# Performance work log

Measured on AMD Instinct MI355X. Metric: run time of the kernel, lower is better.

The kernel has to match this reference:

```python
import jax, jax.numpy as jnp
import numpy as np

B, C, N = 4, 512, 2048
H, DK = 8, 64  # n_heads, d_k; H*DK == C


def setup_inputs() -> dict:
    key = jax.random.key(0)
    k1, k2, k3 = jax.random.split(key, 3)
    x = jax.random.normal(k1, (B, C, N), dtype=jnp.float32)
    # Linear(C, 3*H*DK) and Linear(H*DK, C); torch Linear weight is [out, in]
    Wp = jax.random.normal(k2, (3 * H * DK, C), dtype=jnp.float32) * (C ** -0.5)
    bp = jnp.zeros((3 * H * DK,), dtype=jnp.float32)
    Wo = jax.random.normal(k3, (C, H * DK), dtype=jnp.float32) * ((H * DK) ** -0.5)
    bo = jnp.zeros((C,), dtype=jnp.float32)
    return {"x": x, "Wp": Wp, "bp": bp, "Wo": Wo, "bo": bo}


def reference(x, Wp, bp, Wo, bo):
    b, c, n = x.shape
    scale = DK ** -0.5
    xt = jnp.transpose(x, (0, 2, 1))                    # [b, n, c]
    # NOTE: original forward never applies self.norm (GroupNorm) — faithful omission.
    qkv = xt @ Wp.T + bp                                # [b, n, 3*H*DK]
    qkv = qkv.reshape(b, n, H, 3 * DK)
    q, k, v = jnp.split(qkv, 3, axis=-1)                # each [b, n, H, DK]
    attn = jnp.einsum('bihd,bjhd->bijh', q, k) * scale  # [b, n, n, H]
    attn = jax.nn.softmax(attn, axis=1)                 # softmax over QUERY axis (nonstandard)
    res = jnp.einsum('bijh,bjhd->bihd', attn, v)        # [b, n, H, DK]
    res = res.reshape(b, n, H * DK)
    res = res @ Wo.T + bo                               # [b, n, c]
    res = res + xt                                      # shortcut = Identity (in==out)
    return jnp.transpose(res, (0, 2, 1)).reshape(b, c, n)
```

## Files before the change

### kernel.cpp

```cpp
#include <hip/hip_runtime.h>
#include <cstddef>

typedef unsigned short ushort_t;
typedef __attribute__((ext_vector_type(8))) short sh8;
typedef __attribute__((ext_vector_type(4))) float f4;
typedef __attribute__((ext_vector_type(4))) unsigned short us4;

static constexpr int Bc = 4, Cc = 512, Nc = 2048, Hc = 8, DKc = 64, O3c = 1536;
static constexpr int BHN = Bc * Hc * Nc;
static constexpr int NSPLIT_S = 2;
static constexpr float K2 = 0.125f * 1.44269504089f;

__device__ __forceinline__ unsigned short f2bf(float f) {
    union { float f; unsigned u; } v; v.f = f;
    unsigned r = v.u + 0x7FFFu + ((v.u >> 16) & 1u);
    return (unsigned short)(r >> 16);
}
__device__ __forceinline__ float bf2f(unsigned short b) {
    union { unsigned u; float f; } v; v.u = ((unsigned)b) << 16;
    return v.f;
}
__device__ __forceinline__ float ubf(unsigned u) {
    union { unsigned u; float f; } v; v.u = u; return v.f;
}
__device__ __forceinline__ float fexp2(float s) {
    return ubf((unsigned)(int)fmaf(s, 8388608.0f, 1065353216.0f));
}
__device__ __forceinline__ int fexp2_bf(float s) {
    return (int)fmaf(s, 128.0f, 16256.5f);
}
__device__ __forceinline__ void gl_lds16(const ushort_t* g, ushort_t* l) {
    __builtin_amdgcn_global_load_lds(
        (const __attribute__((address_space(1))) unsigned int*)g,
        (__attribute__((address_space(3))) unsigned int*)l, 16, 0, 0);
}

__global__ __launch_bounds__(256) void xpose_kernel(
    const float* __restrict__ x, ushort_t* __restrict__ xt)
{
    __shared__ float t[32][33];
    const int b = blockIdx.z, n0 = blockIdx.x * 32, c0 = blockIdx.y * 32;
    const int tx = threadIdx.x & 31, ty = threadIdx.x >> 5;
    const float* xb = x + (size_t)b * Cc * Nc;
#pragma unroll
    for (int r = 0; r < 4; ++r)
        t[ty + r * 8][tx] = xb[(size_t)(c0 + ty + r * 8) * Nc + n0 + tx];
    __syncthreads();
    ushort_t* xtb = xt + (size_t)b * Nc * Cc;
#pragma unroll
    for (int r = 0; r < 4; ++r)
        xtb[(size_t)(n0 + ty + r * 8) * Cc + c0 + tx] = f2bf(t[tx][ty + r * 8]);
}

__global__ __launch_bounds__(256) void cvt_kernel(
    const float* __restrict__ s, ushort_t* __restrict__ d, int n4)
{
    int i = blockIdx.x * 256 + threadIdx.x;
    if (i < n4) {
        float4 v = ((const float4*)s)[i];
        us4 o = { f2bf(v.x), f2bf(v.y), f2bf(v.z), f2bf(v.w) };
        ((us4*)d)[i] = o;
    }
}

__global__ __launch_bounds__(256) void qkv_kernel(
    const ushort_t* __restrict__ xt, const ushort_t* __restrict__ Wpb,
    const float* __restrict__ bp,
    ushort_t* __restrict__ q, ushort_t* __restrict__ k, ushort_t* __restrict__ vT)
{
    const int tid = threadIdx.x;
    const int wave = tid >> 6, lane = tid & 63, quad = lane >> 4, l15 = lane & 15;
    const int b = blockIdx.z;
    const int m0 = blockIdx.y * 128 + (wave & 1) * 64;
    const int o0 = blockIdx.x * 128 + (wave >> 1) * 64;
    const ushort_t* A  = xt  + ((size_t)b * Nc + m0) * Cc;
    const ushort_t* Bp = Wpb + (size_t)o0 * Cc;

    const int f  = (o0 >> 6) % 3;
    const int h  = o0 / 192;
    const int bh = b * Hc + h;

    f4 acc[4][4];
#pragma unroll
    for (int i = 0; i < 4; ++i)
#pragma unroll
        for (int j = 0; j < 4; ++j) acc[i][j] = (f4)0.f;

    if (f == 2) {
        for (int kk = 0; kk < Cc; kk += 32) {
            sh8 a[4], bb[4];
#pragma unroll
            for (int mi = 0; mi < 4; ++mi)
                a[mi] = *(const sh8*)&A[(size_t)(mi * 16 + l15) * Cc + kk + quad * 8];
#pragma unroll
            for (int ni = 0; ni < 4; ++ni)
                bb[ni] = *(const sh8*)&Bp[(size_t)(ni * 16 + l15) * Cc + kk + quad * 8];
#pragma unroll
            for (int mi = 0; mi < 4; ++mi)
#pragma unroll
                for (int ni = 0; ni < 4; ++ni)
                    acc[mi][ni] = __builtin_amdgcn_mfma_f32_16x16x32_bf16(
                        a[mi], bb[ni], acc[mi][ni], 0, 0, 0);
        }
#pragma unroll
        for (int ni = 0; ni < 4; ++ni) {
            const int o = o0 + ni * 16 + l15;
            const int d = o & 63;
            const float bias = bp[o];
            ushort_t* dst = vT + ((size_t)bh * DKc + d) * Nc + m0;
#pragma unroll
            for (int mi = 0; mi < 4; ++mi) {
                us4 pk = { f2bf(acc[mi][ni][0] + bias), f2bf(acc[mi][ni][1] + bias),
                           f2bf(acc[mi][ni][2] + bias), f2bf(acc[mi][ni][3] + bias) };
                *(us4*)&dst[mi * 16 + quad * 4] = pk;
            }
        }
    } else {
        for (int kk = 0; kk < Cc; kk += 32) {
            sh8 a[4], bb[4];
#pragma unroll
            for (int mi = 0; mi < 4; ++mi)
                a[mi] = *(const sh8*)&A[(size_t)(mi * 16 + l15) * Cc + kk + quad * 8];
#pragma unroll
            for (int ni = 0; ni < 4; ++ni)
                bb[ni] = *(const sh8*)&Bp[(size_t)(ni * 16 + l15) * Cc + kk + quad * 8];
#pragma unroll
            for (int mo = 0; mo < 4; ++mo)
#pragma unroll
                for (int nt = 0; nt < 4; ++nt)
                    acc[mo][nt] = __builtin_amdgcn_mfma_f32_16x16x32_bf16(
                        bb[mo], a[nt], acc[mo][nt], 0, 0, 0);
        }
        const float qs = (f == 0) ? K2 : 1.0f;
        ushort_t* dst = (f == 0 ? q : k) + (size_t)bh * Nc * DKc;
#pragma unroll
        for (int mo = 0; mo < 4; ++mo) {
            const int d0 = mo * 16 + quad * 4;
            const float4 b4 = *(const float4*)&bp[o0 + d0];
#pragma unroll
            for (int nt = 0; nt < 4; ++nt) {
                const int token = m0 + nt * 16 + l15;
                us4 pk = { f2bf((acc[mo][nt][0] + b4.x) * qs),
                           f2bf((acc[mo][nt][1] + b4.y) * qs),
                           f2bf((acc[mo][nt][2] + b4.z) * qs),
                           f2bf((acc[mo][nt][3] + b4.w) * qs) };
                *(us4*)&dst[(size_t)token * DKc + d0] = pk;
            }
        }
    }
}

__global__ __launch_bounds__(256, 2) void stats_kernel(
    const ushort_t* __restrict__ q, const ushort_t* __restrict__ k,
    float* __restrict__ spart)
{
    const int tid = threadIdx.x;
    const int wave = tid >> 6, lane = tid & 63, quad = lane >> 4, l15 = lane & 15;
    const int id = blockIdx.x;
    const int jb = id >> 6;
    const int bh = (id & 63) >> 1;
    const int js = id & 1;
    const int j0 = jb * 256 + wave * 64;
    const int ibase = js * (Nc / NSPLIT_S);
    const ushort_t* K = k + ((size_t)bh * Nc + j0) * DKc;
    const ushort_t* Q = q + (size_t)bh * Nc * DKc;

    sh8 aK[4][2];
#pragma unroll
    for (int mj = 0; mj < 4; ++mj)
#pragma unroll
        for (int kk = 0; kk < 2; ++kk)
            aK[mj][kk] = *(const sh8*)&K[(size_t)(mj * 16 + l15) * DKc + kk * 32 + quad * 8];

    float lsum[4][4] = {};
    for (int it = 0; it < Nc / NSPLIT_S; it += 64) {
        const int i0 = ibase + it;
        sh8 bQ[4][2];
#pragma unroll
        for (int ni = 0; ni < 4; ++ni)
#pragma unroll
            for (int kk = 0; kk < 2; ++kk)
                bQ[ni][kk] = *(const sh8*)&Q[(size_t)(i0 + ni * 16 + l15) * DKc + kk * 32 + quad * 8];
#pragma unroll
        for (int mj = 0; mj < 4; ++mj)
#pragma unroll
            for (int ni = 0; ni < 4; ++ni) {
                f4 s = (f4)0.f;
                s = __builtin_amdgcn_mfma_f32_16x16x32_bf16(aK[mj][0], bQ[ni][0], s, 0, 0, 0);
                s = __builtin_amdgcn_mfma_f32_16x16x32_bf16(aK[mj][1], bQ[ni][1], s, 0, 0, 0);
#pragma unroll
                for (int r = 0; r < 4; ++r)
                    lsum[mj][r] += fexp2(s[r]);
            }
    }
#pragma unroll
    for (int mj = 0; mj < 4; ++mj)
#pragma unroll
        for (int r = 0; r < 4; ++r) {
            float v = lsum[mj][r];
            v += __shfl_xor(v, 1); v += __shfl_xor(v, 2);
            v += __shfl_xor(v, 4); v += __shfl_xor(v, 8);
            if (l15 == 0)
                spart[((size_t)js * Bc * Hc + bh) * Nc + j0 + mj * 16 + quad * 4 + r] = v;
        }
}

__global__ __launch_bounds__(256) void vscale_kernel(
    ushort_t* __restrict__ vT, const float* __restrict__ spart)
{
    int i = blockIdx.x * 256 + threadIdx.x;
    int f = i * 4;
    int row = f >> 11;
    int j = f & 2047;
    int bh = row >> 6;
    const float* sp = spart + (size_t)bh * Nc + j;
    float4 s0 = *(const float4*)sp;
    float4 s1 = *(const float4*)(sp + BHN);
    us4 v = ((us4*)vT)[i];
    us4 o = { f2bf(bf2f(v[0]) / (s0.x + s1.x)), f2bf(bf2f(v[1]) / (s0.y + s1.y)),
              f2bf(bf2f(v[2]) / (s0.z + s1.z)), f2bf(bf2f(v[3]) / (s0.w + s1.w)) };
    ((us4*)vT)[i] = o;
}

__global__ __launch_bounds__(256, 2) void apply_kernel(
    const ushort_t* __restrict__ q, const ushort_t* __restrict__ k,
    const ushort_t* __restrict__ vT,
    ushort_t* __restrict__ part0, ushort_t* __restrict__ part1)
{
    __shared__ __align__(16) ushort_t Ks[128 * 64];
    __shared__ __align__(16) ushort_t Vs[64 * 128];
    __shared__ __align__(16) ushort_t Ps[4][64 * 64];
    const int tid = threadIdx.x;
    const int wave = tid >> 6, lane = tid & 63, quad = lane >> 4, l15 = lane & 15;
    const int id = blockIdx.x;
    const int ibk = id >> 6;
    const int bh = (id & 63) >> 1;
    const int js = id & 1;
    const int b = bh >> 3, h = bh & 7;
    const int i0 = ibk * 256 + wave * 64;
    const int jbase = js * (Nc / 2);
    const ushort_t* Q  = q  + ((size_t)bh * Nc + i0) * DKc;
    const ushort_t* Kb = k  + (size_t)bh * Nc * DKc;
    const ushort_t* Vb = vT + (size_t)bh * DKc * Nc;
    ushort_t* Pw = Ps[wave];
    const int sw = l15 & 7;
    const int hb = (l15 >> 3) & 1;

    sh8 bQ[4][2];
#pragma unroll
    for (int ni = 0; ni < 4; ++ni)
#pragma unroll
        for (int kk = 0; kk < 2; ++kk)
            bQ[ni][kk] = *(const sh8*)&Q[(size_t)(ni * 16 + l15) * DKc + kk * 32 + quad * 8];

    f4 acc[4][4];
#pragma unroll
    for (int i = 0; i < 4; ++i)
#pragma unroll
        for (int j = 0; j < 4; ++j) acc[i][j] = (f4)0.f;

    int koff[4], voff[4], lbase[4];
#pragma unroll
    for (int c = 0; c < 4; ++c) {
        int g = c * 256 + tid;
        int rk = g >> 3, ck = (g & 7) ^ (rk & 7);
        koff[c] = rk * DKc + ck * 8;
        int rv = g >> 4, cs = g & 15, cn = (cs & 8) | ((cs & 7) ^ (rv & 7));
        voff[c] = rv * Nc + cn * 8;
        lbase[c] = (c * 256 + wave * 64) * 8;
    }

    for (int st = 0; st < 8; ++st) {
        const int j0 = jbase + st * 128;
#pragma unroll
        for (int c = 0; c < 4; ++c) {
            gl_lds16(Kb + (size_t)j0 * DKc + koff[c], Ks + lbase[c]);
            gl_lds16(Vb + voff[c] + j0,               Vs + lbase[c]);
        }
        __syncthreads();

#pragma unroll
        for (int jj = 0; jj < 128; jj += 64) {
            sh8 aK[4][2];
#pragma unroll
            for (int mj = 0; mj < 4; ++mj)
#pragma unroll
                for (int kk = 0; kk < 2; ++kk)
                    aK[mj][kk] = *(const sh8*)&Ks[(jj + mj * 16 + l15) * 64 +
                                                  (((kk * 4 + quad) ^ sw) << 3)];
#pragma unroll
            for (int ni = 0; ni < 4; ++ni) {
                const int prow = ni * 16 + l15;
#pragma unroll
                for (int mj = 0; mj < 4; ++mj) {
                    f4 s = (f4)0.f;
                    s = __builtin_amdgcn_mfma_f32_16x16x32_bf16(aK[mj][0], bQ[ni][0], s, 0, 0, 0);
                    s = __builtin_amdgcn_mfma_f32_16x16x32_bf16(aK[mj][1], bQ[ni][1], s, 0, 0, 0);
                    const int e0 = fexp2_bf(s[0]);
                    const int e1 = fexp2_bf(s[1]);
                    const int e2 = fexp2_bf(s[2]);
                    const int e3 = fexp2_bf(s[3]);
                    uint2 pk;
                    pk.x = __builtin_amdgcn_perm((unsigned)e1, (unsigned)e0, 0x05040100u);
                    pk.y = __builtin_amdgcn_perm((unsigned)e3, (unsigned)e2, 0x05040100u);
                    const int off = prow * 64 + ((((mj * 2 + (quad >> 1)) ^ sw)) << 3)
                                  + (((quad & 1) ^ hb) << 2);
                    *(uint2*)&Pw[off] = pk;
                }
            }
#pragma unroll
            for (int kk = 0; kk < 2; ++kk) {
                const int cgk = (((kk * 4 + quad) ^ sw)) << 3;
                const int h0 = hb << 2, h1 = 4 - h0;
                sh8 aP[4], bV[4];
#pragma unroll
                for (int mi = 0; mi < 4; ++mi) {
                    union { sh8 s8; uint2 u[2]; } t;
                    const int rb = (mi * 16 + l15) * 64 + cgk;
                    t.u[0] = *(const uint2*)&Pw[rb + h0];
                    t.u[1] = *(const uint2*)&Pw[rb + h1];
                    aP[mi] = t.s8;
                }
                const int gnat = (jj >> 3) + kk * 4 + quad;
                const int vcg = ((gnat & 8) | ((gnat & 7) ^ sw)) << 3;
#pragma unroll
                for (int nd = 0; nd < 4; ++nd)
                    bV[nd] = *(const sh8*)&Vs[(nd * 16 + l15) * 128 + vcg];
#pragma unroll
                for (int mi = 0; mi < 4; ++mi)
#pragma unroll
                    for (int nd = 0; nd < 4; ++nd)
                        acc[mi][nd] = __builtin_amdgcn_mfma_f32_16x16x32_bf16(
                            aP[mi], bV[nd], acc[mi][nd], 0, 0, 0);
            }
        }
        __syncthreads();
    }

    ushort_t* part = js ? part1 : part0;
    ushort_t* dst = part + ((size_t)b * Nc + i0) * Cc + h * DKc;
#pragma unroll
    for (int mi = 0; mi < 4; ++mi)
#pragma unroll
        for (int nd = 0; nd < 4; ++nd)
#pragma unroll
            for (int r = 0; r < 4; ++r)
                dst[(size_t)(mi * 16 + quad * 4 + r) * Cc + nd * 16 + l15] =
                    f2bf(acc[mi][nd][r]);
}

__global__ __launch_bounds__(256) void reduce_kernel(
    const ushort_t* __restrict__ p0, ushort_t* __restrict__ p1res)
{
    int i = blockIdx.x * 256 + threadIdx.x;
    us4 a = ((const us4*)p0)[i];
    us4 b = ((const us4*)p1res)[i];
    us4 o;
#pragma unroll
    for (int j = 0; j < 4; ++j)
        o[j] = f2bf(bf2f(a[j]) + bf2f(b[j]));
    ((us4*)p1res)[i] = o;
}

__global__ __launch_bounds__(256) void out_kernel(
    const ushort_t* __restrict__ res, const ushort_t* __restrict__ Wob,
    const float* __restrict__ bo, const float* __restrict__ x,
    float* __restrict__ out)
{
    const int tid = threadIdx.x;
    const int wave = tid >> 6, lane = tid & 63, quad = lane >> 4, l15 = lane & 15;
    const int m0  = blockIdx.x * 128 + (wave & 1) * 64;
    const int co0 = blockIdx.y * 128 + (wave >> 1) * 64;
    const ushort_t* A  = res + (size_t)m0 * Cc;
    const ushort_t* Bw = Wob + (size_t)co0 * Cc;

    f4 acc[4][4];
#pragma unroll
    for (int i = 0; i < 4; ++i)
#pragma unroll
        for (int j = 0; j < 4; ++j) acc[i][j] = (f4)0.f;

    for (int kk = 0; kk < Cc; kk += 32) {
        sh8 a[4], bb[4];
#pragma unroll
        for (int mi = 0; mi < 4; ++mi)
            a[mi] = *(const sh8*)&A[(size_t)(mi * 16 + l15) * Cc + kk + quad * 8];
#pragma unroll
        for (int ni = 0; ni < 4; ++ni)
            bb[ni] = *(const sh8*)&Bw[(size_t)(ni * 16 + l15) * Cc + kk + quad * 8];
#pragma unroll
        for (int mi = 0; mi < 4; ++mi)
#pragma unroll
            for (int ni = 0; ni < 4; ++ni)
                acc[mi][ni] = __builtin_amdgcn_mfma_f32_16x16x32_bf16(
                    a[mi], bb[ni], acc[mi][ni], 0, 0, 0);
    }

    const int b = m0 >> 11;
    const int n_base = m0 & 2047;
#pragma unroll
    for (int ni = 0; ni < 4; ++ni) {
        const int co = co0 + ni * 16 + l15;
        const float bias = bo[co];
#pragma unroll
        for (int mi = 0; mi < 4; ++mi) {
            const int n = n_base + mi * 16 + quad * 4;
            const size_t idx = ((size_t)b * Cc + co) * Nc + n;
            float4 xr = *(const float4*)&x[idx];
            float4 o;
            o.x = acc[mi][ni][0] + bias + xr.x;
            o.y = acc[mi][ni][1] + bias + xr.y;
            o.z = acc[mi][ni][2] + bias + xr.z;
            o.w = acc[mi][ni][3] + bias + xr.w;
            *(float4*)&out[idx] = o;
        }
    }
}

extern "C" void kernel_launch(void* const* d_in, const int* in_sizes, int n_in,
                              void* d_out, int out_size, void* d_ws, size_t ws_size,
                              hipStream_t stream)
{
    const float* x  = (const float*)d_in[0];
    const float* Wp = (const float*)d_in[1];
    const float* bp = (const float*)d_in[2];
    const float* Wo = (const float*)d_in[3];
    const float* bo = (const float*)d_in[4];
    float* out = (float*)d_out;

    float* coef  = (float*)d_ws;
    float* spart = coef + BHN;
    ushort_t* wsb = (ushort_t*)(spart + (size_t)NSPLIT_S * BHN);
    const size_t nE = (size_t)Bc * Nc * Cc;
    ushort_t* xt  = wsb;
    ushort_t* Wpb = xt  + nE;
    ushort_t* Wob = Wpb + (size_t)O3c * Cc;
    ushort_t* qw  = Wob + (size_t)Cc * Cc;
    ushort_t* kw  = qw + nE;
    ushort_t* vT  = kw + nE;
    ushort_t* res = vT + nE;

    xpose_kernel<<<dim3(Nc / 32, Cc / 32, Bc), 256, 0, stream>>>(x, xt);
    cvt_kernel<<<dim3((O3c * Cc / 4 + 255) / 256), 256, 0, stream>>>(Wp, Wpb, O3c * Cc / 4);
    cvt_kernel<<<dim3((Cc * Cc / 4 + 255) / 256), 256, 0, stream>>>(Wo, Wob, Cc * Cc / 4);
    qkv_kernel<<<dim3(O3c / 128, Nc / 128, Bc), 256, 0, stream>>>(xt, Wpb, bp, qw, kw, vT);
    stats_kernel<<<dim3(512), 256, 0, stream>>>(qw, kw, spart);
    vscale_kernel<<<dim3((int)(nE / 4 / 256)), 256, 0, stream>>>(vT, spart);
    apply_kernel<<<dim3(512), 256, 0, stream>>>(qw, kw, vT, xt, res);
    reduce_kernel<<<dim3((int)(nE / 4 / 256)), 256, 0, stream>>>(xt, res);
    out_kernel<<<dim3(Bc * Nc / 128, Cc / 128), 256, 0, stream>>>(res, Wob, bo, x, out);
}
```

Measured before the change: 231.0 us.

## Stage QKV GEMM tiles through swizzled LDS with direct global-to-LDS loads

The QKV projection GEMM used to have each wave read its A and B fragments straight from global memory, so the four waves of a block fetched overlapping rows separately. It now loads shared 128x64 tiles of xt and Wp into LDS with gl_lds16 (global-to-LDS), using an XOR swizzle to avoid bank conflicts. All waves then read their MFMA operands from LDS. The aim is to cut redundant global traffic and improve reuse, at the cost of two barriers per K-step and no double buffering. It also sets launch bounds to 2 blocks per CU.

Measured after the change: 202.6 us. 1.14x faster.

```diff
diff --git a/kernel.cpp b/kernel.cpp
--- a/kernel.cpp
+++ b/kernel.cpp
@@ -63,22 +63,27 @@
     }
 }
 
-__global__ __launch_bounds__(256) void qkv_kernel(
+__global__ __launch_bounds__(256, 2) void qkv_kernel(
     const ushort_t* __restrict__ xt, const ushort_t* __restrict__ Wpb,
     const float* __restrict__ bp,
     ushort_t* __restrict__ q, ushort_t* __restrict__ k, ushort_t* __restrict__ vT)
 {
+    __shared__ __align__(16) ushort_t As[128 * 64];
+    __shared__ __align__(16) ushort_t Bs[128 * 64];
     const int tid = threadIdx.x;
     const int wave = tid >> 6, lane = tid & 63, quad = lane >> 4, l15 = lane & 15;
     const int b = blockIdx.z;
-    const int m0 = blockIdx.y * 128 + (wave & 1) * 64;
-    const int o0 = blockIdx.x * 128 + (wave >> 1) * 64;
-    const ushort_t* A  = xt  + ((size_t)b * Nc + m0) * Cc;
-    const ushort_t* Bp = Wpb + (size_t)o0 * Cc;
-
+    const int t0  = blockIdx.y * 128;
+    const int o0b = blockIdx.x * 128;
+    const int wt = wave & 1, wo = wave >> 1;
+    const int m0 = t0 + wt * 64;
+    const int o0 = o0b + wo * 64;
+    const ushort_t* Ag = xt  + ((size_t)b * Nc + t0) * Cc;
+    const ushort_t* Bg = Wpb + (size_t)o0b * Cc;
     const int f  = (o0 >> 6) % 3;
     const int h  = o0 / 192;
     const int bh = b * Hc + h;
+    const int sw = l15 & 7;
 
     f4 acc[4][4];
 #pragma unroll
@@ -86,22 +91,60 @@
 #pragma unroll
         for (int j = 0; j < 4; ++j) acc[i][j] = (f4)0.f;
 
+    int goff[4], lbase[4];
+#pragma unroll
+    for (int c = 0; c < 4; ++c) {
+        int g = c * 256 + tid;
+        int r = g >> 3, cn = (g & 7) ^ (r & 7);
+        goff[c]  = r * Cc + cn * 8;
+        lbase[c] = (c * 256 + wave * 64) * 8;
+    }
+
+    for (int st = 0; st < 8; ++st) {
+        const int k0 = st * 64;
+#pragma unroll
+        for (int c = 0; c < 4; ++c) {
+            gl_lds16(Ag + k0 + goff[c], As + lbase[c]);
+            gl_lds16(Bg + k0 + goff[c], Bs + lbase[c]);
+        }
+        __syncthreads();
+
+        sh8 aA[4][2], bB[4][2];
+#pragma unroll
+        for (int mi = 0; mi < 4; ++mi)
+#pragma unroll
+            for (int kk = 0; kk < 2; ++kk)
+                aA[mi][kk] = *(const sh8*)&As[(wt * 64 + mi * 16 + l15) * 64 +
+                                              (((kk * 4 + quad) ^ sw) << 3)];
+#pragma unroll
+        for (int ni = 0; ni < 4; ++ni)
+#pragma unroll
+            for (int kk = 0; kk < 2; ++kk)
+                bB[ni][kk] = *(const sh8*)&Bs[(wo * 64 + ni * 16 + l15) * 64 +
+                                              (((kk * 4 + quad) ^ sw) << 3)];
+        if (f == 2) {
+#pragma unroll
+            for (int kk = 0; kk < 2; ++kk)
+#pragma unroll
+                for (int mi = 0; mi < 4; ++mi)
+#pragma unroll
+                    for (int ni = 0; ni < 4; ++ni)
+                        acc[mi][ni] = __builtin_amdgcn_mfma_f32_16x16x32_bf16(
+                            aA[mi][kk], bB[ni][kk], acc[mi][ni], 0, 0, 0);
+        } else {
+#pragma unroll
+            for (int kk = 0; kk < 2; ++kk)
+#pragma unroll
+                for (int mo = 0; mo < 4; ++mo)
+#pragma unroll
+                    for (int nt = 0; nt < 4; ++nt)
+                        acc[mo][nt] = __builtin_amdgcn_mfma_f32_16x16x32_bf16(
+                            bB[mo][kk], aA[nt][kk], acc[mo][nt], 0, 0, 0);
+        }
+        __syncthreads();
+    }
+
     if (f == 2) {
-        for (int kk = 0; kk < Cc; kk += 32) {
-            sh8 a[4], bb[4];
-#pragma unroll
-            for (int mi = 0; mi < 4; ++mi)
-                a[mi] = *(const sh8*)&A[(size_t)(mi * 16 + l15) * Cc + kk + quad * 8];
-#pragma unroll
-            for (int ni = 0; ni < 4; ++ni)
-                bb[ni] = *(const sh8*)&Bp[(size_t)(ni * 16 + l15) * Cc + kk + quad * 8];
-#pragma unroll
-            for (int mi = 0; mi < 4; ++mi)
-#pragma unroll
-                for (int ni = 0; ni < 4; ++ni)
-                    acc[mi][ni] = __builtin_amdgcn_mfma_f32_16x16x32_bf16(
-                        a[mi], bb[ni], acc[mi][ni], 0, 0, 0);
-        }
 #pragma unroll
         for (int ni = 0; ni < 4; ++ni) {
             const int o = o0 + ni * 16 + l15;
@@ -116,21 +159,6 @@
             }
         }
     } else {
-        for (int kk = 0; kk < Cc; kk += 32) {
-            sh8 a[4], bb[4];
-#pragma unroll
-            for (int mi = 0; mi < 4; ++mi)
-                a[mi] = *(const sh8*)&A[(size_t)(mi * 16 + l15) * Cc + kk + quad * 8];
-#pragma unroll
-            for (int ni = 0; ni < 4; ++ni)
-                bb[ni] = *(const sh8*)&Bp[(size_t)(ni * 16 + l15) * Cc + kk + quad * 8];
-#pragma unroll
-            for (int mo = 0; mo < 4; ++mo)
-#pragma unroll
-                for (int nt = 0; nt < 4; ++nt)
-                    acc[mo][nt] = __builtin_amdgcn_mfma_f32_16x16x32_bf16(
-                        bb[mo], a[nt], acc[mo][nt], 0, 0, 0);
-        }
         const float qs = (f == 0) ? K2 : 1.0f;
         ushort_t* dst = (f == 0 ? q : k) + (size_t)bh * Nc * DKc;
 #pragma unroll
```
